# Kernel optimization log

Measured on AMD Instinct MI355X. Metric: run time of the kernel, lower is better.

Reference implementation:

```python
import jax, jax.numpy as jnp
import numpy as np

B, H, S, DH = 1, 16, 4096, 128
D_MODEL = H * DH  # 2048


def setup_inputs() -> dict:
    key = jax.random.key(0)
    kq, kk, kv = jax.random.split(key, 3)
    q = jax.random.normal(kq, (B, H, S, DH), dtype=jnp.float32)
    k = jax.random.normal(kk, (B, H, S, DH), dtype=jnp.float32)
    v = jax.random.normal(kv, (B, H, S, DH), dtype=jnp.float32)
    # causal mask: 1 where attending is allowed, 0 elsewhere (masked_fill on ==0)
    attn_mask = jnp.tril(jnp.ones((S, S), dtype=jnp.int32))[None, None, :, :]
    return {"q": q, "k": k, "v": v, "seq_length": S, "attn_mask": attn_mask}


def reference(q, k, v, seq_length, attn_mask):
    # q,k,v: [1, H, S, DH]; attn_mask: [1, 1, S, S] (0 = masked)
    scale = 1.0 / jnp.sqrt(jnp.asarray(q.shape[-1], dtype=q.dtype))
    att = jnp.einsum("bhqd,bhkd->bhqk", q, k) * scale  # [1,H,S,S]
    mask = attn_mask[:, :, :seq_length, :seq_length]
    att = jnp.where(mask == 0, jnp.asarray(-jnp.inf, dtype=att.dtype), att)
    att = jax.nn.softmax(att, axis=-1)
    y = jnp.einsum("bhqk,bhkd->bhqd", att, v)  # [1,H,S,DH]
    # transpose(1,2) -> [1,S,H,DH] -> view(S, d_model)
    y = jnp.transpose(y, (0, 2, 1, 3)).reshape(seq_length, H * DH)
    return y
```

## Files before the change

### kernel.cpp

```cpp
#include <hip/hip_runtime.h>

#define HH 16
#define SS 4096
#define DHD 128
#define BR 64
#define BC 64
#define LDQ 144
#define LDV 68
#define LDPT 72
#define LDOS 136
#define DM  (HH * DHD)

typedef __bf16 bf16x8_t __attribute__((ext_vector_type(8)));
typedef __bf16 bf16x4_t __attribute__((ext_vector_type(4)));
typedef float  f32x4_t  __attribute__((ext_vector_type(4)));

#define BAR() asm volatile("s_waitcnt lgkmcnt(0)\n\ts_barrier" ::: "memory")

__device__ __forceinline__ f32x4_t vmax4(f32x4_t a, f32x4_t b) {
    f32x4_t r;
    r[0] = fmaxf(a[0], b[0]); r[1] = fmaxf(a[1], b[1]);
    r[2] = fmaxf(a[2], b[2]); r[3] = fmaxf(a[3], b[3]);
    return r;
}

__global__ __launch_bounds__(256, 2)
void fa_fwd(const float* __restrict__ q, const float* __restrict__ k,
            const float* __restrict__ v, float* __restrict__ out)
{
    const int L = blockIdx.x;
    const int h = L & 15;
    const int g = L >> 4;
    const int qts[2] = { g, 63 - g };

    const int tid  = threadIdx.x;
    const int wave = tid >> 6;
    const int lane = tid & 63;
    const int l16  = lane & 15;
    const int quad = lane >> 4;
    const int rK   = tid >> 5;
    const int c4   = tid & 31;
    const int dbase = (wave & 1) * 64;
    const int rbase = (wave >> 1) * 32;

    __shared__ __align__(16) char smem[63488];
    unsigned short* qp_s = (unsigned short*)smem;
    unsigned short* k_s  = (unsigned short*)(smem + 18432);
    unsigned short* vt_s = (unsigned short*)(smem + 36864);
    unsigned short* pT_s = (unsigned short*)(smem + 54272);
    float* os = (float*)smem;

    const size_t hoff = (size_t)h * SS * DHD;
    const float* qh = q + hoff;
    const float* kh = k + hoff;
    const float* vh = v + hoff;

    float4 kreg[8];
    float  vreg[8][4];
    auto issue = [&](int j) {
        const float* kb = kh + (size_t)j * BC * DHD;
        #pragma unroll
        for (int i = 0; i < 8; ++i)
            kreg[i] = ((const float4*)(kb + (size_t)(rK + i * 8) * DHD))[c4];
        const float* vb = vh + (size_t)j * BC * DHD + dbase + lane;
        #pragma unroll
        for (int p = 0; p < 8; ++p) {
            const float* vp = vb + (size_t)(rbase + p * 4) * DHD;
            vreg[p][0] = vp[0];
            vreg[p][1] = vp[DHD];
            vreg[p][2] = vp[2 * DHD];
            vreg[p][3] = vp[3 * DHD];
        }
    };

    const float scale = 0.088388347648318447f;
    issue(0);

    for (int t = 0; t < 2; ++t) {
        const int qt = qts[t];
        __syncthreads();
        #pragma unroll
        for (int i = 0; i < 8; ++i) {
            int idx = tid + i * 256;
            int r   = idx >> 5;
            int cc  = idx & 31;
            float4 val = ((const float4*)(qh + (size_t)(qt * BR + r) * DHD))[cc];
            bf16x4_t bb;
            bb[0] = (__bf16)(val.x * scale); bb[1] = (__bf16)(val.y * scale);
            bb[2] = (__bf16)(val.z * scale); bb[3] = (__bf16)(val.w * scale);
            *(bf16x4_t*)&qp_s[r * LDQ + cc * 4] = bb;
        }
        __syncthreads();

        bf16x8_t qf[4];
        #pragma unroll
        for (int kc = 0; kc < 4; ++kc)
            qf[kc] = *(const bf16x8_t*)
                &qp_s[(wave * 16 + l16) * LDQ + kc * 32 + quad * 8];

        f32x4_t oacc[8];
        #pragma unroll
        for (int mt = 0; mt < 8; ++mt) oacc[mt] = (f32x4_t)(0.0f);
        float mi = -INFINITY, li = 0.0f;

        const int q_local = wave * 16 + l16;

        for (int j = 0; j <= qt; ++j) {
            BAR();
            #pragma unroll
            for (int i = 0; i < 8; ++i) {
                bf16x4_t bb;
                bb[0] = (__bf16)kreg[i].x; bb[1] = (__bf16)kreg[i].y;
                bb[2] = (__bf16)kreg[i].z; bb[3] = (__bf16)kreg[i].w;
                *(bf16x4_t*)&k_s[(rK + i * 8) * LDQ + c4 * 4] = bb;
            }
            #pragma unroll
            for (int p = 0; p < 8; ++p) {
                bf16x4_t bb;
                bb[0] = (__bf16)vreg[p][0]; bb[1] = (__bf16)vreg[p][1];
                bb[2] = (__bf16)vreg[p][2]; bb[3] = (__bf16)vreg[p][3];
                *(bf16x4_t*)&vt_s[(dbase + lane) * LDV + rbase + p * 4] = bb;
            }
            if (j < qt)      issue(j + 1);
            else if (t == 0) issue(0);
            BAR();

            f32x4_t sa[4];
            #pragma unroll
            for (int mt = 0; mt < 4; ++mt) sa[mt] = (f32x4_t)(0.0f);
            #pragma unroll
            for (int kc = 0; kc < 4; ++kc)
                #pragma unroll
                for (int mt = 0; mt < 4; ++mt) {
                    bf16x8_t kf = *(const bf16x8_t*)
                        &k_s[(mt * 16 + l16) * LDQ + kc * 32 + quad * 8];
                    sa[mt] = __builtin_amdgcn_mfma_f32_16x16x32_bf16(kf, qf[kc], sa[mt], 0, 0, 0);
                }

            if (j == qt) {
                #pragma unroll
                for (int mt = 0; mt < 4; ++mt)
                    #pragma unroll
                    for (int r = 0; r < 4; ++r)
                        if (mt * 16 + quad * 4 + r > q_local) sa[mt][r] = -INFINITY;
            }

            f32x4_t mv = vmax4(vmax4(sa[0], sa[1]), vmax4(sa[2], sa[3]));
            float mx = fmaxf(fmaxf(mv[0], mv[1]), fmaxf(mv[2], mv[3]));
            mx = fmaxf(mx, __shfl_xor(mx, 16));
            mx = fmaxf(mx, __shfl_xor(mx, 32));
            float mnew = fmaxf(mi, mx);
            float a = __expf(mi - mnew);
            mi = mnew;
            bf16x4_t pkv[4];
            #pragma unroll
            for (int mt = 0; mt < 4; ++mt) {
                #pragma unroll
                for (int r = 0; r < 4; ++r) sa[mt][r] = __expf(sa[mt][r] - mnew);
                pkv[mt][0] = (__bf16)sa[mt][0]; pkv[mt][1] = (__bf16)sa[mt][1];
                pkv[mt][2] = (__bf16)sa[mt][2]; pkv[mt][3] = (__bf16)sa[mt][3];
            }
            f32x4_t sv = sa[0] + sa[1] + sa[2] + sa[3];
            float rs = (sv[0] + sv[1]) + (sv[2] + sv[3]);
            rs += __shfl_xor(rs, 16);
            rs += __shfl_xor(rs, 32);
            li = li * a + rs;

            #pragma unroll
            for (int mt = 0; mt < 4; ++mt)
                *(bf16x4_t*)&pT_s[(wave * 16 + l16) * LDPT + mt * 16 + quad * 4] = pkv[mt];

            #pragma unroll
            for (int mt = 0; mt < 8; ++mt) {
                oacc[mt][0] *= a; oacc[mt][1] *= a;
                oacc[mt][2] *= a; oacc[mt][3] *= a;
            }

            #pragma unroll
            for (int kc = 0; kc < 2; ++kc) {
                bf16x8_t pb = *(const bf16x8_t*)
                    &pT_s[(wave * 16 + l16) * LDPT + kc * 32 + quad * 8];
                #pragma unroll
                for (int mt = 0; mt < 8; ++mt) {
                    bf16x4_t vlo = *(const bf16x4_t*)
                        &vt_s[(mt * 16 + l16) * LDV + kc * 32 + quad * 8];
                    bf16x4_t vhi = *(const bf16x4_t*)
                        &vt_s[(mt * 16 + l16) * LDV + kc * 32 + quad * 8 + 4];
                    bf16x8_t vf = __builtin_shufflevector(vlo, vhi, 0,1,2,3,4,5,6,7);
                    oacc[mt] = __builtin_amdgcn_mfma_f32_16x16x32_bf16(vf, pb, oacc[mt], 0, 0, 0);
                }
            }
        }

        __syncthreads();
        float inv = 1.0f / li;
        #pragma unroll
        for (int mt = 0; mt < 8; ++mt)
            #pragma unroll
            for (int r = 0; r < 4; ++r)
                os[(wave * 16 + l16) * LDOS + mt * 16 + quad * 4 + r] = oacc[mt][r] * inv;
        __syncthreads();
        #pragma unroll
        for (int p = 0; p < 8; ++p) {
            int row = p * 8 + rK;
            float4 f4 = *(const float4*)&os[row * LDOS + c4 * 4];
            *(float4*)&out[(size_t)(qt * BR + row) * DM + h * DHD + c4 * 4] = f4;
        }
    }
}

extern "C" void kernel_launch(void* const* d_in, const int* in_sizes, int n_in,
                              void* d_out, int out_size, void* d_ws, size_t ws_size,
                              hipStream_t stream) {
    const float* q = (const float*)d_in[0];
    const float* k = (const float*)d_in[1];
    const float* v = (const float*)d_in[2];
    float* out = (float*)d_out;
    fa_fwd<<<dim3((SS / BR / 2) * HH), dim3(256), 0, stream>>>(q, k, v, out);
}
```

Before: 291.9 us.

## Pre-convert K/V to swizzled bf16 tiles and stream via direct global-to-LDS loads

Adds two prep kernels that convert K and V into bf16 tiles, with V transposed and both XOR-swizzled, stored in the workspace. The attention kernel then double-buffers these tiles into LDS using global_load_lds, so the per-tile register conversion and transpose stores go away and half as many bytes are read per tile. It also switches to exp2 with a log2e-folded scale, skips rescaling the accumulator when the running max grows by at most 8, and raises wave priority around the MFMA blocks. In exchange there are two extra kernel launches and a workspace round trip, and the path depends on the workspace being large enough, otherwise it falls back to the old kernel.

```diff
diff --git a/kernel.cpp b/kernel.cpp
--- a/kernel.cpp
+++ b/kernel.cpp
@@ -5,6 +5,7 @@
 #define DHD 128
 #define BR 64
 #define BC 64
+#define LDQS 136
 #define LDQ 144
 #define LDV 68
 #define LDPT 72
@@ -15,7 +16,14 @@
 typedef __bf16 bf16x4_t __attribute__((ext_vector_type(4)));
 typedef float  f32x4_t  __attribute__((ext_vector_type(4)));
 
-#define BAR() asm volatile("s_waitcnt lgkmcnt(0)\n\ts_barrier" ::: "memory")
+#define BAR()  asm volatile("s_waitcnt lgkmcnt(0)\n\ts_barrier" ::: "memory")
+#define BARV() asm volatile("s_waitcnt vmcnt(0)\n\ts_barrier" ::: "memory")
+
+typedef __attribute__((address_space(1))) const void gas_t;
+typedef __attribute__((address_space(3))) void las_t;
+__device__ __forceinline__ void gl16(const void* g, void* l) {
+    __builtin_amdgcn_global_load_lds((gas_t*)g, (las_t*)l, 16, 0, 0);
+}
 
 __device__ __forceinline__ f32x4_t vmax4(f32x4_t a, f32x4_t b) {
     f32x4_t r;
@@ -24,9 +32,232 @@
     return r;
 }
 
+__global__ __launch_bounds__(256)
+void prep_k(const float* __restrict__ k, __bf16* __restrict__ wk)
+{
+    const int c0 = (blockIdx.x * 256 + threadIdx.x) * 4;
+    #pragma unroll
+    for (int i = 0; i < 4; ++i) {
+        const int c    = c0 + i;
+        const int tile = c >> 10;
+        const int o    = (c & 1023) * 16;
+        const int row  = o >> 8;
+        const int e0   = (o & 255) >> 1;
+        const int scol = e0 ^ ((row & 7) << 3);
+        const float* src = k + (((size_t)(tile * 64 + row)) << 7) + scol;
+        float4 a = ((const float4*)src)[0];
+        float4 b = ((const float4*)src)[1];
+        bf16x8_t bb;
+        bb[0] = (__bf16)a.x; bb[1] = (__bf16)a.y; bb[2] = (__bf16)a.z; bb[3] = (__bf16)a.w;
+        bb[4] = (__bf16)b.x; bb[5] = (__bf16)b.y; bb[6] = (__bf16)b.z; bb[7] = (__bf16)b.w;
+        *(bf16x8_t*)((char*)wk + (size_t)c * 16) = bb;
+    }
+}
+
+__global__ __launch_bounds__(256)
+void prep_v(const float* __restrict__ v, __bf16* __restrict__ wv)
+{
+    __shared__ __bf16 lt[64 * 132];
+    const int tile = blockIdx.x;
+    const int tid  = threadIdx.x;
+    #pragma unroll
+    for (int i = 0; i < 8; ++i) {
+        int idx = tid + i * 256;
+        int r = idx >> 5, cc = idx & 31;
+        float4 val = ((const float4*)(v + (((size_t)(tile * 64 + r)) << 7)))[cc];
+        bf16x4_t bb;
+        bb[0] = (__bf16)val.x; bb[1] = (__bf16)val.y;
+        bb[2] = (__bf16)val.z; bb[3] = (__bf16)val.w;
+        *(bf16x4_t*)&lt[r * 132 + cc * 4] = bb;
+    }
+    __syncthreads();
+    #pragma unroll
+    for (int i = 0; i < 4; ++i) {
+        int ch = tid * 4 + i;
+        int o  = ch * 8;
+        int d  = o >> 6;
+        int e0 = o & 63;
+        int ks = e0 ^ ((d & 7) << 3);
+        bf16x8_t bb;
+        #pragma unroll
+        for (int z = 0; z < 8; ++z) bb[z] = lt[(ks + z) * 132 + d];
+        *(bf16x8_t*)((char*)wv + (size_t)tile * 16384 + (size_t)o * 2) = bb;
+    }
+}
+
 __global__ __launch_bounds__(256, 2)
-void fa_fwd(const float* __restrict__ q, const float* __restrict__ k,
-            const float* __restrict__ v, float* __restrict__ out)
+void fa_fwd(const float* __restrict__ q, const __bf16* __restrict__ wk,
+            const __bf16* __restrict__ wv, float* __restrict__ out)
+{
+    const int L = blockIdx.x;
+    const int h = L & 15;
+    const int g = L >> 4;
+    const int qts[2] = { g, 63 - g };
+
+    const int tid  = threadIdx.x;
+    const int wave = tid >> 6;
+    const int lane = tid & 63;
+    const int l16  = lane & 15;
+    const int quad = lane >> 4;
+    const int rK   = tid >> 5;
+    const int c4   = tid & 31;
+    const int swz  = (l16 & 7) << 4;
+
+    __shared__ __align__(16) char smem[74752];
+    unsigned short* pT_s = (unsigned short*)(smem + 65536);
+    unsigned short* q_s  = (unsigned short*)(smem + 32768);
+    float* os = (float*)smem;
+
+    const float* qh = q + (size_t)h * SS * DHD;
+
+    auto stage = [&](int j, int b) {
+        const size_t tb = ((size_t)(h * 64 + j)) * 16384;
+        const char* gk = (const char*)wk + tb + wave * 4096 + lane * 16;
+        const char* gv = (const char*)wv + tb + wave * 4096 + lane * 16;
+        char* lk = smem + b * 16384 + wave * 4096;
+        char* lv = smem + 32768 + b * 16384 + wave * 4096;
+        #pragma unroll
+        for (int c2 = 0; c2 < 4; ++c2) {
+            gl16(gk + c2 * 1024, lk + c2 * 1024);
+            gl16(gv + c2 * 1024, lv + c2 * 1024);
+        }
+    };
+
+    const float scale = 0.088388347648318447f * 1.4426950408889634f;
+
+    for (int t = 0; t < 2; ++t) {
+        const int qt = qts[t];
+        __syncthreads();
+        #pragma unroll
+        for (int i = 0; i < 8; ++i) {
+            int idx = tid + i * 256;
+            int r   = idx >> 5;
+            int cc  = idx & 31;
+            float4 val = ((const float4*)(qh + (size_t)(qt * BR + r) * DHD))[cc];
+            bf16x4_t bb;
+            bb[0] = (__bf16)(val.x * scale); bb[1] = (__bf16)(val.y * scale);
+            bb[2] = (__bf16)(val.z * scale); bb[3] = (__bf16)(val.w * scale);
+            *(bf16x4_t*)&q_s[r * LDQS + cc * 4] = bb;
+        }
+        __syncthreads();
+
+        bf16x8_t qf[4];
+        #pragma unroll
+        for (int kc = 0; kc < 4; ++kc)
+            qf[kc] = *(const bf16x8_t*)
+                &q_s[(wave * 16 + l16) * LDQS + kc * 32 + quad * 8];
+        BAR();
+
+        stage(0, 0);
+
+        f32x4_t oacc[8];
+        #pragma unroll
+        for (int mt = 0; mt < 8; ++mt) oacc[mt] = (f32x4_t)(0.0f);
+        float mi = -INFINITY, li = 0.0f;
+
+        const int q_local = wave * 16 + l16;
+
+        for (int j = 0; j <= qt; ++j) {
+            const int cur = j & 1;
+            BARV();
+            if (j < qt) stage(j + 1, cur ^ 1);
+
+            const char* kb = smem + cur * 16384;
+            const char* vb = smem + 32768 + cur * 16384;
+
+            f32x4_t sa[4];
+            #pragma unroll
+            for (int mt = 0; mt < 4; ++mt) sa[mt] = (f32x4_t)(0.0f);
+            __builtin_amdgcn_s_setprio(1);
+            #pragma unroll
+            for (int kc = 0; kc < 4; ++kc)
+                #pragma unroll
+                for (int mt = 0; mt < 4; ++mt) {
+                    bf16x8_t kf = *(const bf16x8_t*)
+                        (kb + (mt * 16 + l16) * 256 + ((kc * 64 + quad * 16) ^ swz));
+                    sa[mt] = __builtin_amdgcn_mfma_f32_16x16x32_bf16(kf, qf[kc], sa[mt], 0, 0, 0);
+                }
+            __builtin_amdgcn_s_setprio(0);
+
+            if (j == qt) {
+                #pragma unroll
+                for (int mt = 0; mt < 4; ++mt)
+                    #pragma unroll
+                    for (int r = 0; r < 4; ++r)
+                        if (mt * 16 + quad * 4 + r > q_local) sa[mt][r] = -INFINITY;
+            }
+
+            f32x4_t mv = vmax4(vmax4(sa[0], sa[1]), vmax4(sa[2], sa[3]));
+            float mx = fmaxf(fmaxf(mv[0], mv[1]), fmaxf(mv[2], mv[3]));
+            mx = fmaxf(mx, __shfl_xor(mx, 16));
+            mx = fmaxf(mx, __shfl_xor(mx, 32));
+            const bool skip = __all((int)(mx <= mi + 8.0f)) != 0;
+            const float mnew = skip ? mi : fmaxf(mi, mx);
+            bf16x4_t pkv[4];
+            #pragma unroll
+            for (int mt = 0; mt < 4; ++mt) {
+                #pragma unroll
+                for (int r = 0; r < 4; ++r)
+                    sa[mt][r] = __builtin_amdgcn_exp2f(sa[mt][r] - mnew);
+                pkv[mt][0] = (__bf16)sa[mt][0]; pkv[mt][1] = (__bf16)sa[mt][1];
+                pkv[mt][2] = (__bf16)sa[mt][2]; pkv[mt][3] = (__bf16)sa[mt][3];
+            }
+            f32x4_t sv = sa[0] + sa[1] + sa[2] + sa[3];
+            float rs = (sv[0] + sv[1]) + (sv[2] + sv[3]);
+            rs += __shfl_xor(rs, 16);
+            rs += __shfl_xor(rs, 32);
+            if (skip) {
+                li += rs;
+            } else {
+                float a = __builtin_amdgcn_exp2f(mi - mnew);
+                mi = mnew;
+                li = li * a + rs;
+                #pragma unroll
+                for (int mt = 0; mt < 8; ++mt) {
+                    oacc[mt][0] *= a; oacc[mt][1] *= a;
+                    oacc[mt][2] *= a; oacc[mt][3] *= a;
+                }
+            }
+
+            #pragma unroll
+            for (int mt = 0; mt < 4; ++mt)
+                *(bf16x4_t*)&pT_s[q_local * LDPT + mt * 16 + quad * 4] = pkv[mt];
+
+            __builtin_amdgcn_s_setprio(1);
+            #pragma unroll
+            for (int kc = 0; kc < 2; ++kc) {
+                bf16x8_t pb = *(const bf16x8_t*)
+                    &pT_s[q_local * LDPT + kc * 32 + quad * 8];
+                #pragma unroll
+                for (int mt = 0; mt < 8; ++mt) {
+                    bf16x8_t vf = *(const bf16x8_t*)
+                        (vb + (mt * 16 + l16) * 128 + ((kc * 64 + quad * 16) ^ swz));
+                    oacc[mt] = __builtin_amdgcn_mfma_f32_16x16x32_bf16(vf, pb, oacc[mt], 0, 0, 0);
+                }
+            }
+            __builtin_amdgcn_s_setprio(0);
+        }
+
+        __syncthreads();
+        float inv = 1.0f / li;
+        #pragma unroll
+        for (int mt = 0; mt < 8; ++mt)
+            #pragma unroll
+            for (int r = 0; r < 4; ++r)
+                os[(wave * 16 + l16) * LDOS + mt * 16 + quad * 4 + r] = oacc[mt][r] * inv;
+        __syncthreads();
+        #pragma unroll
+        for (int p = 0; p < 8; ++p) {
+            int row = p * 8 + rK;
+            float4 f4 = *(const float4*)&os[row * LDOS + c4 * 4];
+            *(float4*)&out[(size_t)(qts[t] * BR + row) * DM + h * DHD + c4 * 4] = f4;
+        }
+    }
+}
+
+__global__ __launch_bounds__(256, 2)
+void fa_fwd_fb(const float* __restrict__ q, const float* __restrict__ k,
+               const float* __restrict__ v, float* __restrict__ out)
 {
     const int L = blockIdx.x;
     const int h = L & 15;
@@ -102,7 +333,6 @@
         #pragma unroll
         for (int mt = 0; mt < 8; ++mt) oacc[mt] = (f32x4_t)(0.0f);
         float mi = -INFINITY, li = 0.0f;
-
         const int q_local = wave * 16 + l16;
 
         for (int j = 0; j <= qt; ++j) {
@@ -216,5 +446,13 @@
     const float* k = (const float*)d_in[1];
     const float* v = (const float*)d_in[2];
     float* out = (float*)d_out;
-    fa_fwd<<<dim3((SS / BR / 2) * HH), dim3(256), 0, stream>>>(q, k, v, out);
-}
+    if (d_ws != nullptr && ws_size >= (size_t)33554432) {
+        __bf16* wk = (__bf16*)d_ws;
+        __bf16* wv = (__bf16*)((char*)d_ws + 16777216);
+        prep_k<<<dim3(1024), dim3(256), 0, stream>>>(k, wk);
+        prep_v<<<dim3(1024), dim3(256), 0, stream>>>(v, wv);
+        fa_fwd<<<dim3((SS / BR / 2) * HH), dim3(256), 0, stream>>>(q, wk, wv, out);
+    } else {
+        fa_fwd_fb<<<dim3((SS / BR / 2) * HH), dim3(256), 0, stream>>>(q, k, v, out);
+    }
+}
```

New measurement: 289.6 us. About the same (-0.8%).
